# Kernel tuning notes

Measured on AMD Instinct MI355X. Metric: run time of the kernel, lower is better.

The kernel has to match this reference:

```python
import jax, jax.numpy as jnp
import numpy as np
import math

BATCH, SEQLEN, HID, STATE = 8, 4096, 1024, 64


def setup_inputs() -> dict:
    key = jax.random.key(0)
    k_u, k_a, k_b, k_c = jax.random.split(key, 4)
    u = jax.random.normal(k_u, (BATCH, SEQLEN, HID), dtype=jnp.float32)
    A = jax.random.normal(k_a, (HID, STATE), dtype=jnp.float32)
    Bm = jax.random.normal(k_b, (HID, STATE), dtype=jnp.float32)
    C = jax.random.normal(k_c, (HID, STATE), dtype=jnp.float32)
    Dv = jnp.zeros((HID,), dtype=jnp.float32)
    # buffer: dt = exp(linspace(log 1e-3, log 1e-1, state_size))
    dt = jnp.exp(jnp.linspace(math.log(0.001), math.log(0.1), STATE)).astype(jnp.float32)
    return {"u": u, "A": A, "Bm": Bm, "C": C, "Dv": Dv, "dt": dt}


def reference(u, A, Bm, C, Dv, dt):
    # Diagonal LTI SSM (ZOH discretization):
    #   A_cont = -exp(A)                         (Dh, N)
    #   dA = exp(A_cont * dt)                    (Dh, N)
    #   dB = Bm * (1 - dA) / (-A_cont)           (Dh, N)
    # recurrence: x_t = x_{t-1} * dA + u_t * dB;  y_t = sum_n C * x_t + Dv * u_t
    Aexp = jnp.exp(A)                 # -A_cont, positive
    dA = jnp.exp(-Aexp * dt[None, :])
    dB = Bm * (1.0 - dA) / Aexp

    B_, L, Dh = u.shape
    N = dA.shape[1]

    def step(x, u_t):
        # x: (B, Dh, N), u_t: (B, Dh)
        x = x * dA + u_t[..., None] * dB
        y = jnp.einsum('bdn,dn->bd', x, C)
        return x, y

    x0 = jnp.zeros((B_, Dh, N), dtype=u.dtype)
    _, ys = jax.lax.scan(step, x0, jnp.swapaxes(u, 0, 1))  # ys: (L, B, Dh)
    out = jnp.swapaxes(ys, 0, 1) + u * Dv[None, None, :]
    return out
```

## Files before the change

kernel.cpp:

```cpp
#include <hip/hip_runtime.h>
#include <math.h>

#define BATCH  8
#define SEQLEN 4096
#define HID    1024
#define STATE  64
#define NC     16
#define TC     (SEQLEN / NC)
#define TT     32
#define NTILE  (TC / TT)
#define DBLK   64
#define NS     16
#define NP     8
#define RB     8

typedef float f32x2 __attribute__((ext_vector_type(2)));

#define WS_PA 0
#define WS_PW (256 * 1024)
#define WS_PE (512 * 1024)
#define WS_ZL (1024 * 1024)

__device__ __forceinline__ void gload_lds16(const float* g, float* l) {
    __builtin_amdgcn_global_load_lds((const __attribute__((address_space(1))) void*)g,
                                     (__attribute__((address_space(3))) void*)l,
                                     16, 0, 0);
}

__device__ __forceinline__ float quad_reduce_add(float y) {
    int t = __builtin_amdgcn_mov_dpp(__builtin_bit_cast(int, y), 0xB1, 0xF, 0xF, true);
    y += __builtin_bit_cast(float, t);
    t = __builtin_amdgcn_mov_dpp(__builtin_bit_cast(int, y), 0x4E, 0xF, 0xF, true);
    y += __builtin_bit_cast(float, t);
    return y;
}

__global__ void k0_params(const float* __restrict__ A, const float* __restrict__ Bm,
                          const float* __restrict__ C, const float* __restrict__ dt,
                          float* __restrict__ pa, float* __restrict__ pw,
                          float* __restrict__ pE) {
    int i = blockIdx.x * 256 + threadIdx.x;
    if (i >= HID * STATE) return;
    int n = i & (STATE - 1);
    float aexp = expf(A[i]);
    float dtn  = dt[n];
    float a    = expf(-aexp * dtn);
    pa[i] = a;
    pw[i] = C[i] * (Bm[i] * (1.0f - a) / aexp);
    pE[i] = expf(-aexp * dtn * (float)TC);
}

__global__ __launch_bounds__(256, 3) void k1_locals(const float* __restrict__ u,
                                                    const float* __restrict__ pa,
                                                    float* __restrict__ zl) {
    __shared__ float utile[2][TT * DBLK];
    int bid  = blockIdx.x;
    int dset = bid & 15;
    int b    = (bid >> 4) & 7;
    int c    = bid >> 7;
    int w    = threadIdx.x >> 6;
    int lane = threadIdx.x & 63;
    int dl   = lane >> 2, p = lane & 3;
    int d    = dset * DBLK + w * 16 + dl;

    f32x2 a2[NP], z2[NP];
    {
        const f32x2* pap = (const f32x2*)(pa + (size_t)d * STATE + p * NS);
        #pragma unroll
        for (int j = 0; j < NP; j++) a2[j] = pap[j];
    }
    #pragma unroll
    for (int j = 0; j < NP; j++) { z2[j].x = 0.f; z2[j].y = 0.f; }

    const char* ubase = (const char*)(u + ((size_t)b * SEQLEN + (size_t)c * TC) * HID
                                        + (size_t)dset * DBLK);

    #define ISSUE_TILE(t, buf)                                                        \
        {                                                                             \
            _Pragma("unroll")                                                         \
            for (int k = 0; k < 2; k++) {                                             \
                int off = w * 2048 + k * 1024 + lane * 16;      \
                int row = off >> 8;                                                   \
                int col = off & 255;                                                  \
                const float* src = (const float*)(ubase + ((size_t)((t) * TT + row)) * (HID * 4) + col); \
                float* dst = &utile[buf][w * 512 + k * 256];                           \
                gload_lds16(src, dst);                                                \
            }                                                                         \
        }

    ISSUE_TILE(0, 0);
    __syncthreads();
    int cur = 0;
    for (int tile = 0; tile < NTILE; ++tile) {
        if (tile + 1 < NTILE) ISSUE_TILE(tile + 1, cur ^ 1);
        const float* ut = &utile[cur][w * 16 + dl];
        #pragma unroll
        for (int r = 0; r < TT; r++) {
            float uss = ut[r * DBLK];
            f32x2 us; us.x = uss; us.y = uss;
            #pragma unroll
            for (int j = 0; j < NP; j++)
                z2[j] = __builtin_elementwise_fma(a2[j], z2[j], us);
        }
        __syncthreads();
        cur ^= 1;
    }

    f32x2* zp = (f32x2*)(zl + (((size_t)c * BATCH + b) * HID + d) * STATE + p * NS);
    #pragma unroll
    for (int j = 0; j < NP; j++) zp[j] = z2[j];
}

__global__ void k2_scan(const float* __restrict__ pE, float* __restrict__ zl) {
    int i  = blockIdx.x * 256 + threadIdx.x;
    int dn = i & (HID * STATE - 1);
    float E = pE[dn];
    size_t stride = (size_t)BATCH * HID * STATE;
    float g = zl[i];
    for (int c = 1; c < NC - 1; c++) {
        float v = zl[i + c * stride];
        g = fmaf(E, g, v);
        zl[i + c * stride] = g;
    }
}

__global__ __launch_bounds__(256, 3) void k3_main(const float* __restrict__ u,
                                                  const float* __restrict__ Dv,
                                                  const float* __restrict__ pa,
                                                  const float* __restrict__ pw,
                                                  const float* __restrict__ zl,
                                                  float* __restrict__ out) {
    __shared__ float utile[2][TT * DBLK];
    int bid  = blockIdx.x;
    int dset = bid & 15;
    int b    = (bid >> 4) & 7;
    int c    = bid >> 7;
    int w    = threadIdx.x >> 6;
    int lane = threadIdx.x & 63;
    int dl   = lane >> 2, p = lane & 3;
    int d    = dset * DBLK + w * 16 + dl;

    f32x2 a2[NP], w2[NP], z2[NP];
    {
        const f32x2* pap = (const f32x2*)(pa + (size_t)d * STATE + p * NS);
        const f32x2* pwp = (const f32x2*)(pw + (size_t)d * STATE + p * NS);
        #pragma unroll
        for (int j = 0; j < NP; j++) { a2[j] = pap[j]; w2[j] = pwp[j]; }
    }
    if (c == 0) {
        #pragma unroll
        for (int j = 0; j < NP; j++) { z2[j].x = 0.f; z2[j].y = 0.f; }
    } else {
        size_t stride = (size_t)BATCH * HID * STATE;
        const f32x2* zp = (const f32x2*)(zl + (size_t)(c - 1) * stride +
                                         ((size_t)b * HID + d) * STATE + p * NS);
        #pragma unroll
        for (int j = 0; j < NP; j++) z2[j] = zp[j];
    }

    float dvd = Dv[d];
    const char* ubase = (const char*)(u + ((size_t)b * SEQLEN + (size_t)c * TC) * HID
                                        + (size_t)dset * DBLK);
    float* po = out + ((size_t)b * SEQLEN + (size_t)c * TC) * HID + d;

    ISSUE_TILE(0, 0);
    __syncthreads();
    int cur = 0;
    for (int tile = 0; tile < NTILE; ++tile) {
        if (tile + 1 < NTILE) ISSUE_TILE(tile + 1, cur ^ 1);
        const float* ut = &utile[cur][w * 16 + dl];
        float* po_t = po + (size_t)tile * TT * HID;
        #pragma unroll
        for (int r0 = 0; r0 < TT; r0 += RB) {
            float ylane[RB], usv[RB];
            #pragma unroll
            for (int i = 0; i < RB; i++) {
                float uss = ut[(r0 + i) * DBLK];
                usv[i] = uss;
                f32x2 us; us.x = uss; us.y = uss;
                #pragma unroll
                for (int j = 0; j < NP; j++)
                    z2[j] = __builtin_elementwise_fma(a2[j], z2[j], us);
                f32x2 acc0 = z2[0] * w2[0];
                f32x2 acc1 = z2[1] * w2[1];
                #pragma unroll
                for (int j = 2; j < NP; j += 2) {
                    acc0 = __builtin_elementwise_fma(z2[j + 0], w2[j + 0], acc0);
                    acc1 = __builtin_elementwise_fma(z2[j + 1], w2[j + 1], acc1);
                }
                acc0 += acc1;
                ylane[i] = acc0.x + acc0.y;
            }
            #pragma unroll
            for (int i = 0; i < RB; i++) ylane[i] = quad_reduce_add(ylane[i]);
            #pragma unroll
            for (int i = 0; i < RB; i++)
                po_t[(size_t)(r0 + i) * HID] = fmaf(dvd, usv[i], ylane[i]);
        }
        __syncthreads();
        cur ^= 1;
    }
}

extern "C" void kernel_launch(void* const* d_in, const int* in_sizes, int n_in,
                              void* d_out, int out_size, void* d_ws, size_t ws_size,
                              hipStream_t stream) {
    const float* u  = (const float*)d_in[0];
    const float* A  = (const float*)d_in[1];
    const float* Bm = (const float*)d_in[2];
    const float* C  = (const float*)d_in[3];
    const float* Dv = (const float*)d_in[4];
    const float* dt = (const float*)d_in[5];
    float* out = (float*)d_out;

    char* ws = (char*)d_ws;
    float* pa = (float*)(ws + WS_PA);
    float* pw = (float*)(ws + WS_PW);
    float* pE = (float*)(ws + WS_PE);
    float* zl = (float*)(ws + WS_ZL);

    k0_params<<<(HID * STATE) / 256, 256, 0, stream>>>(A, Bm, C, dt, pa, pw, pE);
    k1_locals<<<16 * 8 * (NC - 1), 256, 0, stream>>>(u, pa, zl);
    k2_scan<<<(BATCH * HID * STATE) / 256, 256, 0, stream>>>(pE, zl);
    k3_main<<<16 * 8 * NC, 256, 0, stream>>>(u, Dv, pa, pw, zl, out);
}
```

Measured before the change: 173.9 us.

## Replace per-step scan output with bf16 MFMA Toeplitz convolution plus state correction

The main output kernel now treats each 256-step chunk as a causal convolution with a precomputed kernel K[t] = sum_n C·dB·a^t. It runs this as bf16 16x16x32 MFMA products over a reversed Toeplitz layout. The carried-in chunk state is added through a second MFMA against precomputed W2 = C·dB·a^(t+1) weights with bf16-converted states. Helper kernels build the kernel, weights and transposed states. This trades the scalar per-step FMA recurrence for tensor-core matrix work, at the cost of bf16 precision loss on the inputs and kernels, about 85MB of workspace, and a fallback path when the workspace is too small.

```diff
diff --git a/kernel.cpp b/kernel.cpp
--- a/kernel.cpp
+++ b/kernel.cpp
@@ -15,11 +15,24 @@
 #define RB     8
 
 typedef float f32x2 __attribute__((ext_vector_type(2)));
-
-#define WS_PA 0
-#define WS_PW (256 * 1024)
-#define WS_PE (512 * 1024)
-#define WS_ZL (1024 * 1024)
+typedef float f32x4 __attribute__((ext_vector_type(4)));
+typedef short bf16x8 __attribute__((ext_vector_type(8)));
+typedef short bf16x8u __attribute__((ext_vector_type(8), aligned(4)));
+
+#define WS_PA  0
+#define WS_PW  (256 * 1024)
+#define WS_PE  (512 * 1024)
+#define WS_KR  (1024 * 1024)
+#define WS_ZL  (4  * 1024 * 1024)
+#define WS_ZT  (36 * 1024 * 1024)
+#define WS_W2  (52 * 1024 * 1024)
+#define WS_NEED (85ull * 1024 * 1024)
+
+__device__ __forceinline__ unsigned short f2bf(float x) {
+    unsigned int u = __builtin_bit_cast(unsigned int, x);
+    u = (u + 0x7FFFu + ((u >> 16) & 1u)) >> 16;
+    return (unsigned short)u;
+}
 
 __device__ __forceinline__ void gload_lds16(const float* g, float* l) {
     __builtin_amdgcn_global_load_lds((const __attribute__((address_space(1))) void*)g,
@@ -50,6 +63,39 @@
     pE[i] = expf(-aexp * dtn * (float)TC);
 }
 
+__global__ void k_kr(const float* __restrict__ pa, const float* __restrict__ pw,
+                     const float* __restrict__ Dv, unsigned short* __restrict__ KR2) {
+    __shared__ float K[256];
+    int d = blockIdx.x, n = threadIdx.x;
+    float a = pa[d * 64 + n];
+    float v = pw[d * 64 + n];
+    float dvd = Dv[d];
+    for (int t = 0; t < 256; t++) {
+        float s = v;
+        #pragma unroll
+        for (int off = 1; off < 64; off <<= 1) s += __shfl_xor(s, off);
+        if (n == 0) K[t] = s + (t == 0 ? dvd : 0.0f);
+        v *= a;
+    }
+    __syncthreads();
+    unsigned short* kd = KR2 + (size_t)d * 1056;
+    for (int i = n; i < 528; i += 64) {
+        int x0 = 255 - i;
+        int x1 = 254 - i;
+        kd[i]       = (x0 >= 0) ? f2bf(K[x0]) : 0;
+        kd[528 + i] = (x1 >= 0) ? f2bf(K[x1]) : 0;
+    }
+}
+
+__global__ void k_w2(const float* __restrict__ pa, const float* __restrict__ pw,
+                     unsigned short* __restrict__ W2) {
+    int d = blockIdx.x, n = threadIdx.x;
+    float a = pa[d * 64 + n];
+    float v = pw[d * 64 + n] * a;
+    unsigned short* wd = W2 + (size_t)d * 256 * 64 + n;
+    for (int t = 0; t < 256; t++) { wd[(size_t)t * 64] = f2bf(v); v *= a; }
+}
+
 __global__ __launch_bounds__(256, 3) void k1_locals(const float* __restrict__ u,
                                                     const float* __restrict__ pa,
                                                     float* __restrict__ zl) {
@@ -79,7 +125,7 @@
         {                                                                             \
             _Pragma("unroll")                                                         \
             for (int k = 0; k < 2; k++) {                                             \
-                int off = w * 2048 + k * 1024 + lane * 16;      \
+                int off = w * 2048 + k * 1024 + lane * 16;                            \
                 int row = off >> 8;                                                   \
                 int col = off & 255;                                                  \
                 const float* src = (const float*)(ubase + ((size_t)((t) * TT + row)) * (HID * 4) + col); \
@@ -124,12 +170,125 @@
     }
 }
 
-__global__ __launch_bounds__(256, 3) void k3_main(const float* __restrict__ u,
-                                                  const float* __restrict__ Dv,
-                                                  const float* __restrict__ pa,
-                                                  const float* __restrict__ pw,
-                                                  const float* __restrict__ zl,
+__global__ void k_zt(const float* __restrict__ zl, unsigned short* __restrict__ ZT) {
+    int idx = blockIdx.x * 256 + threadIdx.x;
+    int n  = idx & 63;
+    int bc = (idx >> 6) & 127;
+    int d  = idx >> 13;
+    int b = bc >> 4, c = bc & 15;
+    float z = 0.0f;
+    if (c > 0)
+        z = zl[((size_t)((c - 1) * 8 + b) * 1024 + d) * 64 + n];
+    ZT[idx] = f2bf(z);
+}
+
+__global__ __launch_bounds__(512, 2) void k3_mfma(const float* __restrict__ u,
+                                                  const unsigned short* __restrict__ KR2,
+                                                  const unsigned short* __restrict__ W2,
+                                                  const unsigned short* __restrict__ ZT,
                                                   float* __restrict__ out) {
+    __shared__ float ulds[2][32 * 256];
+    int bid = blockIdx.x;
+    int dg  = bid & 63;
+    int bcg = (bid >> 6) & 7;
+    int th  = bid >> 9;
+    int tid = threadIdx.x;
+    int w   = tid >> 6;
+    int l   = tid & 63;
+    int g   = l >> 4;
+    int r16 = l & 15;
+
+    int bcs = l >> 2;
+    int dqs = (l & 3) ^ (bcs & 3);
+    int bs  = (bcg * 16 + bcs) >> 4;
+    int cs  = (bcg * 16 + bcs) & 15;
+    const float* ubase = u + ((size_t)bs * SEQLEN + (size_t)cs * TC) * HID
+                           + dg * 16 + dqs * 4;
+
+    int nslab = 4 + 4 * th;
+
+    f32x4 acc[2][8];
+    #pragma unroll
+    for (int dd = 0; dd < 2; dd++)
+        #pragma unroll
+        for (int tt = 0; tt < 8; tt++) { acc[dd][tt] = (f32x4){0.f,0.f,0.f,0.f}; }
+
+    #define K3_STAGE(sk_, buf_)                                                   \
+        {                                                                         \
+            _Pragma("unroll")                                                     \
+            for (int iq = 0; iq < 4; iq++) {                                      \
+                int srow = w * 4 + iq;                                            \
+                gload_lds16(ubase + (size_t)((sk_) * 32 + srow) * HID,            \
+                            &ulds[buf_][srow * 256]);                             \
+            }                                                                     \
+        }
+
+    K3_STAGE(0, 0);
+    __syncthreads();
+
+    int L0 = 255 - th * 128 + 8 * g - r16;
+
+    for (int sk = 0; sk < nslab; sk++) {
+        int cur = sk & 1;
+        if (sk + 1 < nslab) K3_STAGE(sk + 1, cur ^ 1);
+        #pragma unroll
+        for (int dd = 0; dd < 2; dd++) {
+            int dloc = w * 2 + dd;
+            int base_e = r16 * 16 + (((dloc >> 2) ^ (r16 & 3)) << 2) + (dloc & 3) + g * 8 * 256;
+            bf16x8 B;
+            #pragma unroll
+            for (int j = 0; j < 8; j++)
+                B[j] = (short)f2bf(ulds[cur][base_e + j * 256]);
+            const unsigned short* krd = KR2 + (size_t)(dg * 16 + dloc) * 1056;
+            #pragma unroll
+            for (int tt = 0; tt < 8; tt++) {
+                int i0 = L0 + sk * 32 - tt * 16;
+                const unsigned short* ap = krd + (i0 & 1) * 528 + (i0 & ~1);
+                bf16x8 A = (bf16x8)*(const bf16x8u*)ap;
+                acc[dd][tt] = __builtin_amdgcn_mfma_f32_16x16x32_bf16(A, B, acc[dd][tt], 0, 0, 0);
+            }
+        }
+        __syncthreads();
+    }
+
+    #pragma unroll
+    for (int dd = 0; dd < 2; dd++) {
+        int d = dg * 16 + w * 2 + dd;
+        const unsigned short* ztd = ZT + ((size_t)d * 128 + bcg * 16) * 64;
+        const unsigned short* w2d = W2 + ((size_t)d * 256 + th * 128) * 64;
+        #pragma unroll
+        for (int ns = 0; ns < 2; ns++) {
+            bf16x8 Bz = (bf16x8)*(const bf16x8u*)(ztd + (size_t)r16 * 64 + ns * 32 + 8 * g);
+            #pragma unroll
+            for (int tt = 0; tt < 8; tt++) {
+                bf16x8 Aw = (bf16x8)*(const bf16x8u*)(w2d + (size_t)(tt * 16 + r16) * 64 + ns * 32 + 8 * g);
+                acc[dd][tt] = __builtin_amdgcn_mfma_f32_16x16x32_bf16(Aw, Bz, acc[dd][tt], 0, 0, 0);
+            }
+        }
+    }
+
+    int bco = bcg * 16 + r16;
+    int bo  = bco >> 4, co = bco & 15;
+    #pragma unroll
+    for (int dd = 0; dd < 2; dd++) {
+        int d = dg * 16 + w * 2 + dd;
+        #pragma unroll
+        for (int tt = 0; tt < 8; tt++) {
+            #pragma unroll
+            for (int rr = 0; rr < 4; rr++) {
+                int t = th * 128 + tt * 16 + g * 4 + rr;
+                out[((size_t)bo * SEQLEN + (size_t)co * TC + t) * HID + d] = acc[dd][tt][rr];
+            }
+        }
+    }
+}
+
+__global__ __launch_bounds__(256, 3) void k3_scalar(const float* __restrict__ u,
+                                                    const float* __restrict__ Dv,
+                                                    const float* __restrict__ pa,
+                                                    const float* __restrict__ pw,
+                                                    const float* __restrict__ zl,
+                                                    float* __restrict__ out) {
     __shared__ float utile[2][TT * DBLK];
     int bid  = blockIdx.x;
     int dset = bid & 15;
@@ -217,10 +376,21 @@
     float* pa = (float*)(ws + WS_PA);
     float* pw = (float*)(ws + WS_PW);
     float* pE = (float*)(ws + WS_PE);
+    unsigned short* KR2 = (unsigned short*)(ws + WS_KR);
     float* zl = (float*)(ws + WS_ZL);
+    unsigned short* ZT  = (unsigned short*)(ws + WS_ZT);
+    unsigned short* W2  = (unsigned short*)(ws + WS_W2);
 
     k0_params<<<(HID * STATE) / 256, 256, 0, stream>>>(A, Bm, C, dt, pa, pw, pE);
     k1_locals<<<16 * 8 * (NC - 1), 256, 0, stream>>>(u, pa, zl);
     k2_scan<<<(BATCH * HID * STATE) / 256, 256, 0, stream>>>(pE, zl);
-    k3_main<<<16 * 8 * NC, 256, 0, stream>>>(u, Dv, pa, pw, zl, out);
-}
+
+    if (ws_size >= WS_NEED) {
+        k_kr<<<1024, 64, 0, stream>>>(pa, pw, Dv, KR2);
+        k_w2<<<1024, 64, 0, stream>>>(pa, pw, W2);
+        k_zt<<<(1024 * 128 * 64) / 256, 256, 0, stream>>>(zl, ZT);
+        k3_mfma<<<64 * 8 * 2, 512, 0, stream>>>(u, KR2, W2, ZT, out);
+    } else {
+        k3_scalar<<<16 * 8 * NC, 256, 0, stream>>>(u, Dv, pa, pw, zl, out);
+    }
+}
```

Result: slower. 420.7 us (+141.9%).

## Recast chunk output as bf16 MFMA convolution plus state-carry matmul

Applied to the files above, without the earlier changes.

Replaces the per-timestep scalar recurrence in the main kernel with a chunked formulation. Within each chunk the output comes from a Toeplitz convolution with a precomputed impulse-response kernel K. The carried-in state adds through a second decay-weighted matrix. Both are evaluated with bf16 MFMA 16x16x32 instructions, with u converted to bf16 in LDS. New kernels build the bf16 Toeplitz fragments, the W2 fragments and the transposed chunk states. This trades exact fp32 recurrence for tensor-core throughput at bf16 precision, and adds extra setup kernels plus about 148 MB of workspace. It falls back to the old scalar path if the workspace is too small.

```diff
diff --git a/kernel.cpp b/kernel.cpp
--- a/kernel.cpp
+++ b/kernel.cpp
@@ -15,13 +15,27 @@
 #define RB     8
 
 typedef float f32x2 __attribute__((ext_vector_type(2)));
-
-#define WS_PA 0
-#define WS_PW (256 * 1024)
-#define WS_PE (512 * 1024)
-#define WS_ZL (1024 * 1024)
-
-__device__ __forceinline__ void gload_lds16(const float* g, float* l) {
+typedef float f32x4 __attribute__((ext_vector_type(4)));
+typedef short bf16x8 __attribute__((ext_vector_type(8)));
+typedef unsigned int u32x4 __attribute__((ext_vector_type(4)));
+
+#define WS_PA   0
+#define WS_PW   (256 * 1024)
+#define WS_PE   (512 * 1024)
+#define WS_PL2  (768 * 1024)
+#define WS_ZL   (1ull  * 1024 * 1024)
+#define WS_ZT   (36ull * 1024 * 1024)
+#define WS_W2F  (56ull * 1024 * 1024)
+#define WS_KRF  (92ull * 1024 * 1024)
+#define WS_NEED (148ull * 1024 * 1024)
+
+__device__ __forceinline__ unsigned int f2bf(float x) {
+    unsigned int u = __builtin_bit_cast(unsigned int, x);
+    u = (u + 0x7FFFu + ((u >> 16) & 1u)) >> 16;
+    return u & 0xFFFFu;
+}
+
+__device__ __forceinline__ void gload_lds16(const void* g, void* l) {
     __builtin_amdgcn_global_load_lds((const __attribute__((address_space(1))) void*)g,
                                      (__attribute__((address_space(3))) void*)l,
                                      16, 0, 0);
@@ -38,16 +52,17 @@
 __global__ void k0_params(const float* __restrict__ A, const float* __restrict__ Bm,
                           const float* __restrict__ C, const float* __restrict__ dt,
                           float* __restrict__ pa, float* __restrict__ pw,
-                          float* __restrict__ pE) {
+                          float* __restrict__ pE, float* __restrict__ pl2) {
     int i = blockIdx.x * 256 + threadIdx.x;
     if (i >= HID * STATE) return;
     int n = i & (STATE - 1);
     float aexp = expf(A[i]);
     float dtn  = dt[n];
     float a    = expf(-aexp * dtn);
-    pa[i] = a;
-    pw[i] = C[i] * (Bm[i] * (1.0f - a) / aexp);
-    pE[i] = expf(-aexp * dtn * (float)TC);
+    pa[i]  = a;
+    pw[i]  = C[i] * (Bm[i] * (1.0f - a) / aexp);
+    pE[i]  = expf(-aexp * dtn * (float)TC);
+    pl2[i] = -aexp * dtn * 1.44269504088896340736f;
 }
 
 __global__ __launch_bounds__(256, 3) void k1_locals(const float* __restrict__ u,
@@ -79,7 +94,7 @@
         {                                                                             \
             _Pragma("unroll")                                                         \
             for (int k = 0; k < 2; k++) {                                             \
-                int off = w * 2048 + k * 1024 + lane * 16;      \
+                int off = w * 2048 + k * 1024 + lane * 16;                            \
                 int row = off >> 8;                                                   \
                 int col = off & 255;                                                  \
                 const float* src = (const float*)(ubase + ((size_t)((t) * TT + row)) * (HID * 4) + col); \
@@ -124,12 +139,203 @@
     }
 }
 
-__global__ __launch_bounds__(256, 3) void k3_main(const float* __restrict__ u,
-                                                  const float* __restrict__ Dv,
-                                                  const float* __restrict__ pa,
-                                                  const float* __restrict__ pw,
-                                                  const float* __restrict__ zl,
-                                                  float* __restrict__ out) {
+__global__ void k2_zt(const float* __restrict__ pE, const float* __restrict__ zl,
+                      unsigned short* __restrict__ ZT) {
+    int i = blockIdx.x * 256 + threadIdx.x;
+    int n = i & 63;
+    int d = (i >> 6) & 1023;
+    int b = i >> 16;
+    float E = pE[d * 64 + n];
+    size_t stride = (size_t)BATCH * HID * STATE;
+    unsigned short* zt = ZT + (size_t)d * 8192 + (size_t)b * 1024 + n;
+    zt[0] = 0;
+    float g = zl[i];
+    zt[64] = (unsigned short)f2bf(g);
+    for (int c = 2; c < 16; c++) {
+        g = fmaf(E, g, zl[i + (size_t)(c - 1) * stride]);
+        zt[(size_t)c * 64] = (unsigned short)f2bf(g);
+    }
+}
+
+__global__ void k_krf(const float* __restrict__ pw, const float* __restrict__ pl2,
+                      const float* __restrict__ Dv, unsigned short* __restrict__ KRF) {
+    __shared__ float wv[64], e2[64], K[256];
+    int d = blockIdx.x, t = threadIdx.x;
+    if (t < 64) { wv[t] = pw[d * 64 + t]; e2[t] = pl2[d * 64 + t]; }
+    __syncthreads();
+    float s = 0.0f;
+    for (int n = 0; n < 64; n++) s += wv[n] * exp2f((float)t * e2[n]);
+    if (t == 0) s += Dv[d];
+    K[t] = s;
+    __syncthreads();
+    for (int idx = t; idx < 8192; idx += 256) {
+        int j  = idx & 7;
+        int ll = (idx >> 3) & 63;
+        int m  = idx >> 9;
+        int x  = (ll & 15) - 8 * (ll >> 4) + 16 * m - j;
+        unsigned short v = 0;
+        if (x >= 0) v = (unsigned short)f2bf(K[x]);
+        KRF[(size_t)d * 8192 + idx] = v;
+    }
+}
+
+__global__ void k_w2f(const float* __restrict__ pw, const float* __restrict__ pl2,
+                      unsigned short* __restrict__ W2F) {
+    __shared__ float wv[64], e2[64];
+    int d = blockIdx.x, t = threadIdx.x;
+    if (t < 64) { wv[t] = pw[d * 64 + t]; e2[t] = pl2[d * 64 + t]; }
+    __syncthreads();
+    for (int idx = t; idx < 16384; idx += 256) {
+        int j  = idx & 7;
+        int ll = (idx >> 3) & 63;
+        int ns = (idx >> 9) & 1;
+        int tt = idx >> 10;
+        int n  = ns * 32 + 8 * (ll >> 4) + j;
+        int tg = tt * 16 + (ll & 15);
+        float val = wv[n] * exp2f((float)(tg + 1) * e2[n]);
+        W2F[(size_t)d * 16384 + idx] = (unsigned short)f2bf(val);
+    }
+}
+
+__global__ __launch_bounds__(1024, 1) void k3_mfma(const float* __restrict__ u,
+                                                   const unsigned short* __restrict__ KRF,
+                                                   const unsigned short* __restrict__ W2F,
+                                                   const unsigned short* __restrict__ ZT,
+                                                   float* __restrict__ out) {
+    __shared__ __align__(16) char smem[131072];
+    int bid = blockIdx.x;
+    int dg  = bid & 63;
+    int bcg = bid >> 6;
+    int tid = threadIdx.x;
+    int w   = tid >> 6;
+    int l   = tid & 63;
+    int g   = l >> 4, r16 = l & 15;
+    int d   = dg * 16 + w;
+
+    {
+        int dl = tid & 15;
+        int v  = (tid >> 4) & 63;
+        int bc = v & 15;
+        int sq = v >> 4;
+        int gbc = bcg * 16 + bc;
+        int bs = gbc >> 4, cs = gbc & 15;
+        const float* up = u + ((size_t)(bs * SEQLEN + cs * TC + sq * 64)) * HID
+                            + dg * 16 + dl;
+        unsigned int rowb = (unsigned int)(dl * 16 + bc) * 512;
+        #pragma unroll
+        for (int kk = 0; kk < 8; kk++) {
+            float uv[8];
+            #pragma unroll
+            for (int j = 0; j < 8; j++) uv[j] = up[(size_t)(kk * 8 + j) * HID];
+            unsigned int pk[4];
+            #pragma unroll
+            for (int q = 0; q < 4; q++)
+                pk[q] = f2bf(uv[2 * q]) | (f2bf(uv[2 * q + 1]) << 16);
+            int sc   = sq * 8 + kk;
+            int slot = (sc + 4 * (bc & 7) + 5 * dl) & 31;
+            *(u32x4*)(&smem[rowb + slot * 16]) = (u32x4){pk[0], pk[1], pk[2], pk[3]};
+        }
+    }
+    __syncthreads();
+
+    f32x4 acc[16];
+    #pragma unroll
+    for (int tt = 0; tt < 16; tt++) acc[tt] = (f32x4){0.f, 0.f, 0.f, 0.f};
+
+    const unsigned short* krf = KRF + (size_t)d * 8192 + l * 8;
+    unsigned int rowr = (unsigned int)(w * 16 + r16) * 512;
+    int rot = (4 * (r16 & 7) + 5 * w) & 31;
+
+    {
+        bf16x8 Af[8];
+        #pragma unroll
+        for (int mm = 0; mm < 8; mm++)
+            Af[mm] = *(const bf16x8*)(krf + (size_t)mm * 512);
+        #pragma unroll
+        for (int mm = 0; mm < 8; mm++) {
+            #pragma unroll
+            for (int sk = 0; sk < 8; sk++) {
+                if (2 * sk + mm <= 15) {
+                    int slot = ((sk * 4 + g) + rot) & 31;
+                    bf16x8 B = *(const bf16x8*)(&smem[rowr + slot * 16]);
+                    acc[2 * sk + mm] =
+                        __builtin_amdgcn_mfma_f32_16x16x32_bf16(Af[mm], B, acc[2 * sk + mm], 0, 0, 0);
+                }
+            }
+        }
+    }
+    __builtin_amdgcn_sched_barrier(0);
+    {
+        bf16x8 Af[8];
+        #pragma unroll
+        for (int mm = 0; mm < 8; mm++)
+            Af[mm] = *(const bf16x8*)(krf + (size_t)(8 + mm) * 512);
+        #pragma unroll
+        for (int mm = 0; mm < 8; mm++) {
+            #pragma unroll
+            for (int sk = 0; sk < 4; sk++) {
+                if (2 * sk + 8 + mm <= 15) {
+                    int slot = ((sk * 4 + g) + rot) & 31;
+                    bf16x8 B = *(const bf16x8*)(&smem[rowr + slot * 16]);
+                    acc[2 * sk + 8 + mm] =
+                        __builtin_amdgcn_mfma_f32_16x16x32_bf16(Af[mm], B, acc[2 * sk + 8 + mm], 0, 0, 0);
+                }
+            }
+        }
+    }
+    __builtin_amdgcn_sched_barrier(0);
+
+    {
+        const unsigned short* ztd = ZT + (size_t)d * 8192 + (size_t)bcg * 1024;
+        bf16x8 Bz0 = *(const bf16x8*)(ztd + (size_t)r16 * 64 + 0 * 32 + 8 * g);
+        bf16x8 Bz1 = *(const bf16x8*)(ztd + (size_t)r16 * 64 + 1 * 32 + 8 * g);
+        const unsigned short* w2f = W2F + (size_t)d * 16384 + l * 8;
+        #pragma unroll
+        for (int grp = 0; grp < 4; grp++) {
+            bf16x8 Aw[8];
+            #pragma unroll
+            for (int q = 0; q < 8; q++) {
+                int tt = grp * 4 + (q >> 1);
+                int ns = q & 1;
+                Aw[q] = *(const bf16x8*)(w2f + (size_t)(tt * 2 + ns) * 512);
+            }
+            #pragma unroll
+            for (int q = 0; q < 8; q++) {
+                int tt = grp * 4 + (q >> 1);
+                acc[grp * 4 + (q >> 1)] =
+                    __builtin_amdgcn_mfma_f32_16x16x32_bf16(Aw[q], (q & 1) ? Bz1 : Bz0,
+                                                            acc[tt], 0, 0, 0);
+            }
+            __builtin_amdgcn_sched_barrier(0);
+        }
+    }
+
+    float* eps = (float*)smem;
+    int p = tid >> 2, sub = tid & 3;
+    int t16r = p >> 4, bcr = p & 15;
+    int gbcr = bcg * 16 + bcr;
+    int bo = gbcr >> 4, co = gbcr & 15;
+    float* pout = out + ((size_t)(bo * SEQLEN + co * TC + t16r)) * HID + dg * 16 + sub * 4;
+    #pragma unroll
+    for (int tt = 0; tt < 16; tt++) {
+        __syncthreads();
+        #pragma unroll
+        for (int rr = 0; rr < 4; rr++)
+            eps[((g * 4 + rr) * 16 + r16) * 21 + w] = acc[tt][rr];
+        __syncthreads();
+        f32x4 vv;
+        #pragma unroll
+        for (int j = 0; j < 4; j++) vv[j] = eps[p * 21 + sub * 4 + j];
+        *(f32x4*)(pout + (size_t)(tt * 16) * HID) = vv;
+    }
+}
+
+__global__ __launch_bounds__(256, 3) void k3_scalar(const float* __restrict__ u,
+                                                    const float* __restrict__ Dv,
+                                                    const float* __restrict__ pa,
+                                                    const float* __restrict__ pw,
+                                                    const float* __restrict__ zl,
+                                                    float* __restrict__ out) {
     __shared__ float utile[2][TT * DBLK];
     int bid  = blockIdx.x;
     int dset = bid & 15;
@@ -214,13 +420,27 @@
     float* out = (float*)d_out;
 
     char* ws = (char*)d_ws;
-    float* pa = (float*)(ws + WS_PA);
-    float* pw = (float*)(ws + WS_PW);
-    float* pE = (float*)(ws + WS_PE);
-    float* zl = (float*)(ws + WS_ZL);
-
-    k0_params<<<(HID * STATE) / 256, 256, 0, stream>>>(A, Bm, C, dt, pa, pw, pE);
+    float* pa  = (float*)(ws + WS_PA);
+    float* pw  = (float*)(ws + WS_PW);
+    float* pE  = (float*)(ws + WS_PE);
+    float* pl2 = (float*)(ws + WS_PL2);
+    float* zl  = (float*)(ws + WS_ZL);
+    unsigned short* ZT  = (unsigned short*)(ws + WS_ZT);
+    unsigned short* W2F = (unsigned short*)(ws + WS_W2F);
+    unsigned short* KRF = (unsigned short*)(ws + WS_KRF);
+
+    bool mfma = (ws_size >= WS_NEED);
+
+    k0_params<<<(HID * STATE) / 256, 256, 0, stream>>>(A, Bm, C, dt, pa, pw, pE, pl2);
     k1_locals<<<16 * 8 * (NC - 1), 256, 0, stream>>>(u, pa, zl);
-    k2_scan<<<(BATCH * HID * STATE) / 256, 256, 0, stream>>>(pE, zl);
-    k3_main<<<16 * 8 * NC, 256, 0, stream>>>(u, Dv, pa, pw, zl, out);
-}
+
+    if (mfma) {
+        k_krf<<<1024, 256, 0, stream>>>(pw, pl2, Dv, KRF);
+        k_w2f<<<1024, 256, 0, stream>>>(pw, pl2, W2F);
+        k2_zt<<<(BATCH * HID * STATE) / 256, 256, 0, stream>>>(pE, zl, ZT);
+        k3_mfma<<<512, 1024, 0, stream>>>(u, KRF, W2F, ZT, out);
+    } else {
+        k2_scan<<<(BATCH * HID * STATE) / 256, 256, 0, stream>>>(pE, zl);
+        k3_scalar<<<16 * 8 * NC, 256, 0, stream>>>(u, Dv, pa, pw, zl, out);
+    }
+}
```

New measurement: 180.2 us. 1.04x slower.
